# Kernel optimization log

Measured on AMD Instinct MI355X. Metric: run time of the kernel, lower is better.

The kernel has to match this reference:

```python
import jax, jax.numpy as jnp
import numpy as np

N_LAYERS = 4
D_MODEL = 256
P = 128            # ssm_size // 2 (conj_sym S5)
LATENT_DIM = 256
MAX_SEQ_LEN = 32768
OUTPUT_DIM = 64
LN_EPS = 1e-6      # flax nn.LayerNorm default


def layer_norm(x, scale, bias):
    mu = jnp.mean(x, axis=-1, keepdims=True)
    var = jnp.mean(jnp.square(x - mu), axis=-1, keepdims=True)
    return (x - mu) * jax.lax.rsqrt(var + LN_EPS) * scale + bias


def s5_ssm(u, Lre, Lim, Bre, Bim, Cre, Cim, Dvec, log_step, resets):
    """u: (L, H) float. Returns (L, H) float. conj_sym S5, zoh discretization."""
    step = jnp.exp(log_step)                       # (P,)
    Lam = Lre + 1j * Lim                           # (P,) complex
    Lam_bar = jnp.exp(Lam * step)                  # (P,)
    B_bar = ((Lam_bar - 1.0) / Lam)[:, None] * (Bre + 1j * Bim)  # (P, H)
    Bu = u @ B_bar.T                               # (L, P) complex
    A = jnp.broadcast_to(Lam_bar, Bu.shape)        # (L, P)
    c = resets[:, None].astype(u.dtype)            # (L, 1)

    def binop(qi, qj):
        Ai, bi, ci = qi
        Aj, bj, cj = qj
        return (Aj * Ai * (1.0 - cj) + Aj * cj,
                (Aj * bi + bj) * (1.0 - cj) + bj * cj,
                ci * (1.0 - cj) + cj)

    # zero initial hidden state => no prepend needed (identical result)
    _, xs, _ = jax.lax.associative_scan(binop, (A, Bu, c))
    y = 2.0 * jnp.real(xs @ (Cre + 1j * Cim).T)    # (L, H), conj_sym doubling
    return y + u * Dvec


def setup_inputs() -> dict:
    key = jax.random.key(0)
    ks = jax.random.split(key, 16)
    f = jax.random.normal
    return {
        "latent": f(ks[0], (LATENT_DIM,), jnp.float32),
        "W_expand": f(ks[1], (LATENT_DIM, D_MODEL), jnp.float32) / np.sqrt(LATENT_DIM),
        "b_expand": jnp.zeros((D_MODEL,), jnp.float32),
        "norm_scale": jnp.ones((N_LAYERS, D_MODEL), jnp.float32),
        "norm_bias": jnp.zeros((N_LAYERS, D_MODEL), jnp.float32),
        "Lambda_re": -(0.1 + 0.9 * jax.random.uniform(ks[2], (N_LAYERS, P))),
        "Lambda_im": np.pi * f(ks[3], (N_LAYERS, P), jnp.float32),
        "B_re": f(ks[4], (N_LAYERS, P, D_MODEL), jnp.float32) / np.sqrt(D_MODEL),
        "B_im": f(ks[5], (N_LAYERS, P, D_MODEL), jnp.float32) / np.sqrt(D_MODEL),
        "C_re": f(ks[6], (N_LAYERS, D_MODEL, P), jnp.float32) / np.sqrt(P),
        "C_im": f(ks[7], (N_LAYERS, D_MODEL, P), jnp.float32) / np.sqrt(P),
        "D": f(ks[8], (N_LAYERS, D_MODEL), jnp.float32),
        "log_step": jnp.log(jax.random.uniform(ks[9], (N_LAYERS, P), minval=1e-3, maxval=1e-1)),
        "W1": f(ks[10], (N_LAYERS, D_MODEL, D_MODEL), jnp.float32) / np.sqrt(D_MODEL),
        "b1": jnp.zeros((N_LAYERS, D_MODEL), jnp.float32),
        "W2": f(ks[11], (N_LAYERS, D_MODEL, D_MODEL), jnp.float32) / np.sqrt(D_MODEL),
        "b2": jnp.zeros((N_LAYERS, D_MODEL), jnp.float32),
        "W_out": f(ks[12], (D_MODEL, OUTPUT_DIM), jnp.float32) / np.sqrt(D_MODEL),
        "b_out": jnp.zeros((OUTPUT_DIM,), jnp.float32),
        "seq_len": MAX_SEQ_LEN,
    }


def reference(latent, W_expand, b_expand, norm_scale, norm_bias,
              Lambda_re, Lambda_im, B_re, B_im, C_re, C_im, D, log_step,
              W1, b1, W2, b2, W_out, b_out, seq_len):
    # latent_expand + leaky_relu, then broadcast to full trajectory
    x = jax.nn.leaky_relu(latent @ W_expand + b_expand)        # (H,)
    x = jnp.broadcast_to(x[None, :], (MAX_SEQ_LEN, D_MODEL))    # (L, H); batch dim of 1 dropped
    resets = jnp.zeros((MAX_SEQ_LEN,), x.dtype)                 # dones = zeros
    for i in range(N_LAYERS):
        skip = x
        h = layer_norm(x, norm_scale[i], norm_bias[i])          # prenorm
        y = s5_ssm(h, Lambda_re[i], Lambda_im[i], B_re[i], B_im[i],
                   C_re[i], C_im[i], D[i], log_step[i], resets)
        y = layer_norm(y, norm_scale[i], norm_bias[i])          # gtrxl norm (shared params)
        y = jax.nn.gelu(y)
        y = (y @ W1[i] + b1[i]) * jax.nn.sigmoid(y @ W2[i] + b2[i])  # full_glu
        x = skip + y
    return x @ W_out + b_out                                    # (L, output_dim)
```

## Files before the change

### kernel.cpp

```cpp
#include <hip/hip_runtime.h>
#include <stdint.h>

#define LSEQ 32768
#define NCH 512
#define TCH 64

typedef _Float16 half8 __attribute__((ext_vector_type(8)));
typedef _Float16 half4v __attribute__((ext_vector_type(4)));
typedef _Float16 half2v __attribute__((ext_vector_type(2)));
typedef float f32x4 __attribute__((ext_vector_type(4)));
typedef float f32x2 __attribute__((ext_vector_type(2)));

__device__ __forceinline__ float sigmoidf_(float x) { return 1.f / (1.f + __expf(-x)); }
__device__ __forceinline__ float gelu_(float x) {
    float z = 0.7978845608028654f * (x + 0.044715f * x * x * x);
    float e = __expf(2.f * z);
    float t = 1.f - 2.f / (e + 1.f);
    return 0.5f * x * (1.f + t);
}

__device__ __forceinline__ void gll16(const _Float16* gp, _Float16* lp) {
    __builtin_amdgcn_global_load_lds((__attribute__((address_space(1))) void*)gp,
                                     (__attribute__((address_space(3))) void*)lp, 16, 0, 0);
}

__global__ __launch_bounds__(512) void s5_k0a(const float* __restrict__ lre, const float* __restrict__ lim,
                                              const float* __restrict__ lstep,
                                              float* aR, float* aI, float* cbR, float* cbI,
                                              float* aTR, float* aTI, float* alp, float* ralp) {
    int i = threadIdx.x;
    float st = expf(lstep[i]);
    float lr = lre[i] * st, li = lim[i] * st;
    float ea = expf(lr);
    float ar = ea * cosf(li), ai = ea * sinf(li);
    float den = lre[i] * lre[i] + lim[i] * lim[i];
    float nr = ar - 1.f, ni = ai;
    float cr = (nr * lre[i] + ni * lim[i]) / den;
    float ci = (ni * lre[i] - nr * lim[i]) / den;
    float cm = sqrtf(cr * cr + ci * ci);
    float al = sqrtf(2.83f / fmaxf(cm, 1e-8f));
    float eT = expf(lr * (float)TCH);
    aR[i] = ar; aI[i] = ai;
    cbR[i] = cr; cbI[i] = ci;
    aTR[i] = eT * cosf(li * (float)TCH);
    aTI[i] = eT * sinf(li * (float)TCH);
    alp[i] = al; ralp[i] = 1.f / al;
}

__global__ __launch_bounds__(256) void s5_k0b(const float* __restrict__ Bre, const float* __restrict__ Bim,
                                              const float* __restrict__ Cre, const float* __restrict__ Cim,
                                              const float* __restrict__ W1, const float* __restrict__ W2,
                                              const float* __restrict__ b1, const float* __restrict__ b2,
                                              const float* __restrict__ Wout,
                                              const float* __restrict__ cbR, const float* __restrict__ cbI,
                                              const float* __restrict__ alp, const float* __restrict__ ralp,
                                              _Float16* Wbu, _Float16* Wc, _Float16* Wglu,
                                              _Float16* WoutT, float* bglu) {
    int stride = gridDim.x * blockDim.x;
    int tid0 = blockIdx.x * blockDim.x + threadIdx.x;
    for (int i = tid0; i < 262144; i += stride) {
        int l = i >> 16, n = (i >> 8) & 255, k = i & 255;
        int s = n >> 4, lmn = n & 15;
        int p = l * 128 + (s >> 1) * 16 + lmn;
        float re = cbR[p] * Bre[p * 256 + k] - cbI[p] * Bim[p * 256 + k];
        float im = cbR[p] * Bim[p * 256 + k] + cbI[p] * Bre[p * 256 + k];
        Wbu[i] = (_Float16)(((s & 1) ? im : re) * alp[p]);
    }
    for (int i = tid0; i < 262144; i += stride) {
        int l = i >> 16, n = (i >> 8) & 255, k = i & 255;
        int p = k >> 1;
        float base = (k & 1) ? -2.f * Cim[(l * 256 + n) * 128 + p]
                             : 2.f * Cre[(l * 256 + n) * 128 + p];
        Wc[i] = (_Float16)(base * ralp[l * 128 + p]);
    }
    for (int i = tid0; i < 524288; i += stride) {
        int l = i >> 17, n = (i >> 8) & 511, k = i & 255;
        int j = ((n >> 7) << 6) | (((n >> 6) & 1) << 5) | (((n >> 5) & 1) << 4) | (n & 15);
        const float* src = ((n >> 4) & 1) ? W2 : W1;
        Wglu[i] = (_Float16)src[(l * 256 + k) * 256 + j];
    }
    for (int i = tid0; i < 16384; i += stride) {
        int n = i >> 8, k = i & 255;
        WoutT[i] = (_Float16)Wout[k * 64 + n];
    }
    for (int i = tid0; i < 2048; i += stride) {
        int l = i >> 9, n = i & 511;
        int j = ((n >> 7) << 6) | (((n >> 6) & 1) << 5) | (((n >> 5) & 1) << 4) | (n & 15);
        bglu[i] = (((n >> 4) & 1) ? b2 : b1)[l * 256 + j];
    }
}

__global__ __launch_bounds__(256) void s5_k0c(const float* __restrict__ latent, const float* __restrict__ W,
                                              const float* __restrict__ b, _Float16* __restrict__ x0h) {
    __shared__ float lat[256];
    lat[threadIdx.x] = latent[threadIdx.x];
    __syncthreads();
    float s = b[threadIdx.x];
    for (int k = 0; k < 256; ++k) s += lat[k] * W[k * 256 + threadIdx.x];
    x0h[threadIdx.x] = (_Float16)((s > 0.f) ? s : 0.01f * s);
}

__global__ __launch_bounds__(256) void s5_k1_fill(const _Float16* __restrict__ x0h, _Float16* __restrict__ x) {
    int i = blockIdx.x * 256 + threadIdx.x;
    half8 v = *(const half8*)(x0h + (i & 31) * 8);
    *(half8*)(x + i * 8) = v;
}

__global__ __launch_bounds__(512, 1) void s5_k3_lngemm(const _Float16* __restrict__ x,
                                                       const _Float16* __restrict__ Wt,
                                                       const float* __restrict__ gamma,
                                                       const float* __restrict__ beta,
                                                       _Float16* __restrict__ h,
                                                       _Float16* __restrict__ Buh) {
    __shared__ _Float16 sW[128 * 512];
    int tid = threadIdx.x, wid = tid >> 6, lane = tid & 63;
    int lm = lane & 15, quad = lane >> 4;
    int m0 = blockIdx.x * 128;
    int rowb = m0 + wid * 16;

#pragma unroll
    for (int half = 0; half < 2; ++half)
#pragma unroll
        for (int i = 0; i < 8; ++i) {
            int c = i * 8 + wid;
            int ks = c >> 3, n16 = c & 7;
            gll16(Wt + (half * 128 + n16 * 16 + lm) * 256 + ks * 32 + quad * 8,
                  sW + half * 32768 + c * 512);
        }

    int row = rowb + lm;
    half8 af[8];
    {
        half8 xv[8];
#pragma unroll
        for (int ks = 0; ks < 8; ++ks)
            xv[ks] = *(const half8*)(x + row * 256 + ks * 32 + quad * 8);
        float s1 = 0.f, s2 = 0.f;
#pragma unroll
        for (int i = 0; i < 8; ++i)
#pragma unroll
            for (int j = 0; j < 8; ++j) { float t = (float)xv[i][j]; s1 += t; s2 += t * t; }
        s1 += __shfl_xor(s1, 16, 64); s2 += __shfl_xor(s2, 16, 64);
        s1 += __shfl_xor(s1, 32, 64); s2 += __shfl_xor(s2, 32, 64);
        float mu = s1 * (1.f / 256.f);
        float var = s2 * (1.f / 256.f) - mu * mu;
        float rs = rsqrtf(fmaxf(var, 0.f) + 1e-6f);
#pragma unroll
        for (int ks = 0; ks < 8; ++ks) {
            f32x4 g0 = *(const f32x4*)(gamma + ks * 32 + quad * 8);
            f32x4 g1 = *(const f32x4*)(gamma + ks * 32 + quad * 8 + 4);
            f32x4 b0 = *(const f32x4*)(beta + ks * 32 + quad * 8);
            f32x4 b1 = *(const f32x4*)(beta + ks * 32 + quad * 8 + 4);
            half8 o;
#pragma unroll
            for (int j = 0; j < 4; ++j) {
                o[j]     = (_Float16)(((float)xv[ks][j] - mu) * rs * g0[j] + b0[j]);
                o[j + 4] = (_Float16)(((float)xv[ks][j + 4] - mu) * rs * g1[j] + b1[j]);
            }
            af[ks] = o;
            *(half8*)(h + row * 256 + ks * 32 + quad * 8) = o;
        }
    }
    asm volatile("s_waitcnt vmcnt(0)" ::: "memory");
    __syncthreads();

    f32x4 zero = {0.f, 0.f, 0.f, 0.f};
    f32x4 acc[2][8];
#pragma unroll
    for (int hf = 0; hf < 2; ++hf)
#pragma unroll
        for (int nt = 0; nt < 8; ++nt) acc[hf][nt] = zero;

#pragma unroll
    for (int hf = 0; hf < 2; ++hf)
#pragma unroll
        for (int ks = 0; ks < 8; ++ks) {
            half8 bf[8];
#pragma unroll
            for (int nt = 0; nt < 8; ++nt)
                bf[nt] = *(const half8*)(sW + hf * 32768 + (ks * 8 + nt) * 512 + lane * 8);
#pragma unroll
            for (int nt = 0; nt < 8; ++nt)
                acc[hf][nt] = __builtin_amdgcn_mfma_f32_16x16x32_f16(af[ks], bf[nt], acc[hf][nt], 0, 0, 0);
        }

#pragma unroll
    for (int u = 0; u < 8; ++u) {
        int hf = u >> 2, q = u & 3;
        int p = u * 16 + lm;
#pragma unroll
        for (int r = 0; r < 4; ++r) {
            half2v o = {(_Float16)acc[hf][2 * q][r], (_Float16)acc[hf][2 * q + 1][r]};
            *(half2v*)(Buh + (rowb + quad * 4 + r) * 256 + 2 * p) = o;
        }
    }
}

__global__ __launch_bounds__(128, 4) void s5_k4_carry(const _Float16* __restrict__ Bu,
                                                      const float* __restrict__ aR, const float* __restrict__ aI,
                                                      float* __restrict__ carRI) {
    int p = threadIdx.x, c = blockIdx.x;
    int t0 = c * TCH;
    const _Float16* bp = Bu + t0 * 256 + 2 * p;
    half2v hv[TCH];
#pragma unroll
    for (int j = 0; j < TCH; ++j) hv[j] = *(const half2v*)(bp + j * 256);
    float ar = aR[p], ai = aI[p];
    float sr = 0.f, si = 0.f;
#pragma unroll
    for (int j = 0; j < TCH; ++j) {
        float nr = fmaf(ar, sr, fmaf(-ai, si, (float)hv[j][0]));
        float ni = fmaf(ar, si, fmaf(ai, sr, (float)hv[j][1]));
        sr = nr; si = ni;
    }
    *(f32x2*)(carRI + (c * 128 + p) * 2) = f32x2{sr, si};
}

__global__ __launch_bounds__(512, 1) void s5_k7_mega(const _Float16* __restrict__ Bu,
                                                     const float* __restrict__ carRI,
                                                     const _Float16* __restrict__ Wc,
                                                     const _Float16* __restrict__ Wglu,
                                                     const _Float16* __restrict__ h,
                                                     const float* __restrict__ aR, const float* __restrict__ aI,
                                                     const float* __restrict__ aTR, const float* __restrict__ aTI,
                                                     const float* __restrict__ Dv,
                                                     const float* __restrict__ gamma,
                                                     const float* __restrict__ beta,
                                                     const float* __restrict__ bias,
                                                     _Float16* __restrict__ x) {
    __shared__ _Float16 sW[64 * 512];
    __shared__ _Float16 xsT[128 * 256];
    int tid = threadIdx.x, wid = tid >> 6, lane = tid & 63;
    int lm = lane & 15, quad = lane >> 4;
    int m0 = blockIdx.x * 128;
    int rowb = m0 + wid * 16;

    auto stageWc = [&](int half) {
#pragma unroll
        for (int i = 0; i < 8; ++i) {
            int c = i * 8 + wid;
            int ks = c >> 3, n16 = c & 7;
            gll16(Wc + (half * 128 + n16 * 16 + lm) * 256 + ks * 32 + quad * 8, sW + c * 512);
        }
    };
    auto stageWg = [&](int n0) {
#pragma unroll
        for (int i = 0; i < 8; ++i) {
            int c = i * 8 + wid;
            int ks = c >> 3, n16 = c & 7;
            gll16(Wglu + (n0 + n16 * 16 + lm) * 256 + ks * 32 + quad * 8, sW + c * 512);
        }
    };
    stageWc(0);

    if (tid < 256) {
        int cc = tid >> 7, p = tid & 127;
        int cg = blockIdx.x * 2 + cc;
        const _Float16* bp = Bu + (m0 + cc * TCH) * 256 + 2 * p;
        half2v hv[TCH];
#pragma unroll
        for (int j = 0; j < TCH; ++j) hv[j] = *(const half2v*)(bp + j * 256);
        float tr = aTR[p], ti = aTI[p];
        float cr = 0.f, ci = 0.f;
#pragma unroll 8
        for (int i = 0; i < cg; ++i) {
            f32x2 w = *(const f32x2*)(carRI + (i * 128 + p) * 2);
            float nr = fmaf(tr, cr, fmaf(-ti, ci, w[0]));
            float ni = fmaf(tr, ci, fmaf(ti, cr, w[1]));
            cr = nr; ci = ni;
        }
        float ar = aR[p], ai = aI[p];
        float sr = cr, si = ci;
#pragma unroll
        for (int j = 0; j < TCH; ++j) {
            float nr = fmaf(ar, sr, fmaf(-ai, si, (float)hv[j][0]));
            float ni = fmaf(ar, si, fmaf(ai, sr, (float)hv[j][1]));
            sr = nr; si = ni;
            int rl = cc * TCH + j;
            int byte = (4 * p) ^ ((rl & 7) << 4);
            *(half2v*)((char*)xsT + rl * 512 + byte) = half2v{(_Float16)sr, (_Float16)si};
        }
    }
    asm volatile("s_waitcnt vmcnt(0)" ::: "memory");
    __syncthreads();

    int rl = wid * 16 + lm;
    half8 af[8];
#pragma unroll
    for (int ks = 0; ks < 8; ++ks) {
        int b = ks * 64 + quad * 16;
        af[ks] = *(const half8*)((const char*)xsT + rl * 512 + (b ^ ((rl & 7) << 4)));
    }

    f32x4 zero = {0.f, 0.f, 0.f, 0.f};
    f32x4 acc[2][8];
#pragma unroll
    for (int hf = 0; hf < 2; ++hf)
#pragma unroll
        for (int nt = 0; nt < 8; ++nt) acc[hf][nt] = zero;

#pragma unroll
    for (int ks = 0; ks < 8; ++ks) {
        half8 bf[8];
#pragma unroll
        for (int nt = 0; nt < 8; ++nt)
            bf[nt] = *(const half8*)(sW + (ks * 8 + nt) * 512 + lane * 8);
#pragma unroll
        for (int nt = 0; nt < 8; ++nt)
            acc[0][nt] = __builtin_amdgcn_mfma_f32_16x16x32_f16(af[ks], bf[nt], acc[0][nt], 0, 0, 0);
    }
    __syncthreads();
    stageWc(1);
    asm volatile("s_waitcnt vmcnt(0)" ::: "memory");
    __syncthreads();
#pragma unroll
    for (int ks = 0; ks < 8; ++ks) {
        half8 bf[8];
#pragma unroll
        for (int nt = 0; nt < 8; ++nt)
            bf[nt] = *(const half8*)(sW + (ks * 8 + nt) * 512 + lane * 8);
#pragma unroll
        for (int nt = 0; nt < 8; ++nt)
            acc[1][nt] = __builtin_amdgcn_mfma_f32_16x16x32_f16(af[ks], bf[nt], acc[1][nt], 0, 0, 0);
    }

#pragma unroll
    for (int hf = 0; hf < 2; ++hf)
#pragma unroll
        for (int nt = 0; nt < 8; ++nt) {
            int col = hf * 128 + nt * 16 + lm;
            float dv = Dv[col];
#pragma unroll
            for (int r = 0; r < 4; ++r)
                acc[hf][nt][r] += (float)h[(rowb + quad * 4 + r) * 256 + col] * dv;
        }
    float mu[4], rs[4];
#pragma unroll
    for (int r = 0; r < 4; ++r) {
        float a = 0.f, b = 0.f;
#pragma unroll
        for (int hf = 0; hf < 2; ++hf)
#pragma unroll
            for (int nt = 0; nt < 8; ++nt) {
                float v = acc[hf][nt][r];
                a += v; b += v * v;
            }
#pragma unroll
        for (int off = 1; off < 16; off <<= 1) {
            a += __shfl_xor(a, off, 64);
            b += __shfl_xor(b, off, 64);
        }
        float m = a * (1.f / 256.f);
        float var = b * (1.f / 256.f) - m * m;
        mu[r] = m;
        rs[r] = rsqrtf(fmaxf(var, 0.f) + 1e-6f);
    }
#pragma unroll
    for (int hf = 0; hf < 2; ++hf)
#pragma unroll
        for (int nt = 0; nt < 8; ++nt) {
            int col = hf * 128 + nt * 16 + lm;
            float ga = gamma[col], be = beta[col];
#pragma unroll
            for (int r = 0; r < 4; ++r) {
                float hn = (acc[hf][nt][r] - mu[r]) * rs[r] * ga + be;
                int rg = wid * 16 + quad * 4 + r;
                int byte = (2 * col) ^ ((rg & 7) << 4);
                *((_Float16*)((char*)xsT + rg * 512 + byte)) = (_Float16)gelu_(hn);
            }
        }
    __syncthreads();
    stageWg(0);
    half8 ag[8];
#pragma unroll
    for (int ks = 0; ks < 8; ++ks) {
        int b = ks * 64 + quad * 16;
        ag[ks] = *(const half8*)((const char*)xsT + rl * 512 + (b ^ ((rl & 7) << 4)));
    }
    asm volatile("s_waitcnt vmcnt(0)" ::: "memory");
    __syncthreads();

#pragma unroll
    for (int cy = 0; cy < 4; ++cy) {
        f32x4 accg[8];
#pragma unroll
        for (int nt = 0; nt < 8; ++nt) accg[nt] = zero;
#pragma unroll
        for (int ks = 0; ks < 8; ++ks) {
            half8 bf[8];
#pragma unroll
            for (int nt = 0; nt < 8; ++nt)
                bf[nt] = *(const half8*)(sW + (ks * 8 + nt) * 512 + lane * 8);
#pragma unroll
            for (int nt = 0; nt < 8; ++nt)
                accg[nt] = __builtin_amdgcn_mfma_f32_16x16x32_f16(ag[ks], bf[nt], accg[nt], 0, 0, 0);
        }
        int n0 = cy * 128;
        int jbase = (n0 >> 1) + lm;
        _Float16 xold[4][4];
#pragma unroll
        for (int q = 0; q < 4; ++q)
#pragma unroll
            for (int r = 0; r < 4; ++r)
                xold[q][r] = x[(rowb + quad * 4 + r) * 256 + jbase + q * 16];
#pragma unroll
        for (int q = 0; q < 4; ++q) {
            float b1v = bias[n0 + (2 * q) * 16 + lm];
            float b2v = bias[n0 + (2 * q + 1) * 16 + lm];
            int jcol = jbase + q * 16;
#pragma unroll
            for (int r = 0; r < 4; ++r) {
                float u1 = accg[2 * q][r] + b1v;
                float u2 = accg[2 * q + 1][r] + b2v;
                float gl = u1 * sigmoidf_(u2);
                int idx = (rowb + quad * 4 + r) * 256 + jcol;
                x[idx] = (_Float16)((float)xold[q][r] + gl);
            }
        }
        if (cy < 3) {
            __syncthreads();
            stageWg((cy + 1) * 128);
            asm volatile("s_waitcnt vmcnt(0)" ::: "memory");
            __syncthreads();
        }
    }
}

__global__ __launch_bounds__(256, 2) void s5_k9_gemm_out(const _Float16* __restrict__ A,
                                                         const _Float16* __restrict__ Wt,
                                                         const float* __restrict__ bout,
                                                         float* __restrict__ out) {
    __shared__ _Float16 sW[32 * 512];
    int tid = threadIdx.x, wid = tid >> 6, lane = tid & 63;
    int lm = lane & 15, quad = lane >> 4;
    int m0 = blockIdx.x * 128;
#pragma unroll
    for (int i = 0; i < 8; ++i) {
        int c = i * 4 + wid;
        int ks = c >> 2, n16 = c & 3;
        gll16(Wt + (n16 * 16 + lm) * 256 + ks * 32 + quad * 8, sW + c * 512);
    }
    int rowb = m0 + wid * 32;
    half8 af[2][8];
#pragma unroll
    for (int mt = 0; mt < 2; ++mt)
#pragma unroll
        for (int ks = 0; ks < 8; ++ks)
            af[mt][ks] = *(const half8*)(A + (rowb + mt * 16 + lm) * 256 + ks * 32 + quad * 8);
    asm volatile("s_waitcnt vmcnt(0)" ::: "memory");
    __syncthreads();

    f32x4 zero = {0.f, 0.f, 0.f, 0.f};
    f32x4 acc[2][4];
#pragma unroll
    for (int mt = 0; mt < 2; ++mt)
#pragma unroll
        for (int nt = 0; nt < 4; ++nt) acc[mt][nt] = zero;
#pragma unroll
    for (int ks = 0; ks < 8; ++ks) {
        half8 bf[4];
#pragma unroll
        for (int nt = 0; nt < 4; ++nt)
            bf[nt] = *(const half8*)(sW + (ks * 4 + nt) * 512 + lane * 8);
#pragma unroll
        for (int mt = 0; mt < 2; ++mt)
#pragma unroll
            for (int nt = 0; nt < 4; ++nt)
                acc[mt][nt] = __builtin_amdgcn_mfma_f32_16x16x32_f16(af[mt][ks], bf[nt], acc[mt][nt], 0, 0, 0);
    }
#pragma unroll
    for (int mt = 0; mt < 2; ++mt)
#pragma unroll
        for (int nt = 0; nt < 4; ++nt) {
            int col = nt * 16 + lm;
            float bv = bout[col];
#pragma unroll
            for (int r = 0; r < 4; ++r) {
                int row = rowb + mt * 16 + quad * 4 + r;
                out[row * 64 + col] = acc[mt][nt][r] + bv;
            }
        }
}

constexpr size_t OFF_X    = 0;
constexpr size_t OFF_BU   = 33554432;
constexpr size_t OFF_H    = 67108864;
constexpr size_t OFF_WBU  = 100663296;
constexpr size_t OFF_WC   = OFF_WBU + 524288;
constexpr size_t OFF_WGLU = OFF_WC + 524288;
constexpr size_t OFF_WOUT = OFF_WGLU + 1048576;
constexpr size_t OFF_BGLU = OFF_WOUT + 32768;
constexpr size_t OFF_AR   = OFF_BGLU + 8192;
constexpr size_t OFF_AI   = OFF_AR + 2048;
constexpr size_t OFF_CBR  = OFF_AI + 2048;
constexpr size_t OFF_CBI  = OFF_CBR + 2048;
constexpr size_t OFF_ATR  = OFF_CBI + 2048;
constexpr size_t OFF_ATI  = OFF_ATR + 2048;
constexpr size_t OFF_ALP  = OFF_ATI + 2048;
constexpr size_t OFF_RALP = OFF_ALP + 2048;
constexpr size_t OFF_X0H  = OFF_RALP + 2048;
constexpr size_t OFF_CARRI= OFF_X0H + 1024;

extern "C" void kernel_launch(void* const* d_in, const int* in_sizes, int n_in,
                              void* d_out, int out_size, void* d_ws, size_t ws_size,
                              hipStream_t stream) {
    (void)in_sizes; (void)n_in; (void)out_size; (void)ws_size;
    const float* latent    = (const float*)d_in[0];
    const float* W_expand  = (const float*)d_in[1];
    const float* b_expand  = (const float*)d_in[2];
    const float* norm_s    = (const float*)d_in[3];
    const float* norm_b    = (const float*)d_in[4];
    const float* Lre       = (const float*)d_in[5];
    const float* Lim       = (const float*)d_in[6];
    const float* Bre       = (const float*)d_in[7];
    const float* Bim       = (const float*)d_in[8];
    const float* Cre       = (const float*)d_in[9];
    const float* Cim       = (const float*)d_in[10];
    const float* Dv        = (const float*)d_in[11];
    const float* lstep     = (const float*)d_in[12];
    const float* W1        = (const float*)d_in[13];
    const float* b1        = (const float*)d_in[14];
    const float* W2        = (const float*)d_in[15];
    const float* b2        = (const float*)d_in[16];
    const float* Wout      = (const float*)d_in[17];
    const float* bout      = (const float*)d_in[18];

    char* ws = (char*)d_ws;
    _Float16* x    = (_Float16*)(ws + OFF_X);
    _Float16* Buh  = (_Float16*)(ws + OFF_BU);
    _Float16* hbuf = (_Float16*)(ws + OFF_H);
    _Float16* Wbu  = (_Float16*)(ws + OFF_WBU);
    _Float16* Wc   = (_Float16*)(ws + OFF_WC);
    _Float16* Wglu = (_Float16*)(ws + OFF_WGLU);
    _Float16* WoutT= (_Float16*)(ws + OFF_WOUT);
    float* bglu = (float*)(ws + OFF_BGLU);
    float* aR  = (float*)(ws + OFF_AR);
    float* aI  = (float*)(ws + OFF_AI);
    float* cbR = (float*)(ws + OFF_CBR);
    float* cbI = (float*)(ws + OFF_CBI);
    float* aTR = (float*)(ws + OFF_ATR);
    float* aTI = (float*)(ws + OFF_ATI);
    float* alp = (float*)(ws + OFF_ALP);
    float* ralp= (float*)(ws + OFF_RALP);
    _Float16* x0h = (_Float16*)(ws + OFF_X0H);
    float* carRI=(float*)(ws + OFF_CARRI);

    s5_k0a<<<1, 512, 0, stream>>>(Lre, Lim, lstep, aR, aI, cbR, cbI, aTR, aTI, alp, ralp);
    s5_k0b<<<256, 256, 0, stream>>>(Bre, Bim, Cre, Cim, W1, W2, b1, b2, Wout,
                                    cbR, cbI, alp, ralp, Wbu, Wc, Wglu, WoutT, bglu);
    s5_k0c<<<1, 256, 0, stream>>>(latent, W_expand, b_expand, x0h);
    s5_k1_fill<<<4096, 256, 0, stream>>>(x0h, x);

    for (int l = 0; l < 4; ++l) {
        s5_k3_lngemm<<<256, 512, 0, stream>>>(x, Wbu + l * 65536,
                                              norm_s + l * 256, norm_b + l * 256,
                                              hbuf, Buh);
        s5_k4_carry<<<NCH, 128, 0, stream>>>(Buh, aR + l * 128, aI + l * 128, carRI);
        s5_k7_mega<<<256, 512, 0, stream>>>(Buh, carRI, Wc + l * 65536, Wglu + l * 131072,
                                            hbuf,
                                            aR + l * 128, aI + l * 128,
                                            aTR + l * 128, aTI + l * 128,
                                            Dv + l * 256,
                                            norm_s + l * 256, norm_b + l * 256,
                                            bglu + l * 512, x);
    }
    s5_k9_gemm_out<<<256, 256, 0, stream>>>(x, WoutT, bout, (float*)d_out);
}
```

Baseline: 461.1 us.

## Fuse chunk-carry scan into LN+Bu GEMM kernel via LDS-staged Bu tile

```diff
diff --git a/kernel.cpp b/kernel.cpp
--- a/kernel.cpp
+++ b/kernel.cpp
@@ -110,23 +110,27 @@
                                                        const _Float16* __restrict__ Wt,
                                                        const float* __restrict__ gamma,
                                                        const float* __restrict__ beta,
+                                                       const float* __restrict__ aR,
+                                                       const float* __restrict__ aI,
                                                        _Float16* __restrict__ h,
-                                                       _Float16* __restrict__ Buh) {
-    __shared__ _Float16 sW[128 * 512];
+                                                       _Float16* __restrict__ Buh,
+                                                       float* __restrict__ carRI) {
+    __shared__ _Float16 sW[64 * 512];
+    __shared__ _Float16 BuT[128 * 256];
     int tid = threadIdx.x, wid = tid >> 6, lane = tid & 63;
     int lm = lane & 15, quad = lane >> 4;
     int m0 = blockIdx.x * 128;
     int rowb = m0 + wid * 16;
 
-#pragma unroll
-    for (int half = 0; half < 2; ++half)
+    auto stageW = [&](int half) {
 #pragma unroll
         for (int i = 0; i < 8; ++i) {
             int c = i * 8 + wid;
             int ks = c >> 3, n16 = c & 7;
-            gll16(Wt + (half * 128 + n16 * 16 + lm) * 256 + ks * 32 + quad * 8,
-                  sW + half * 32768 + c * 512);
-        }
+            gll16(Wt + (half * 128 + n16 * 16 + lm) * 256 + ks * 32 + quad * 8, sW + c * 512);
+        }
+    };
+    stageW(0);
 
     int row = rowb + lm;
     half8 af[8];
@@ -172,17 +176,29 @@
         for (int nt = 0; nt < 8; ++nt) acc[hf][nt] = zero;
 
 #pragma unroll
-    for (int hf = 0; hf < 2; ++hf)
-#pragma unroll
-        for (int ks = 0; ks < 8; ++ks) {
-            half8 bf[8];
-#pragma unroll
-            for (int nt = 0; nt < 8; ++nt)
-                bf[nt] = *(const half8*)(sW + hf * 32768 + (ks * 8 + nt) * 512 + lane * 8);
-#pragma unroll
-            for (int nt = 0; nt < 8; ++nt)
-                acc[hf][nt] = __builtin_amdgcn_mfma_f32_16x16x32_f16(af[ks], bf[nt], acc[hf][nt], 0, 0, 0);
-        }
+    for (int ks = 0; ks < 8; ++ks) {
+        half8 bf[8];
+#pragma unroll
+        for (int nt = 0; nt < 8; ++nt)
+            bf[nt] = *(const half8*)(sW + (ks * 8 + nt) * 512 + lane * 8);
+#pragma unroll
+        for (int nt = 0; nt < 8; ++nt)
+            acc[0][nt] = __builtin_amdgcn_mfma_f32_16x16x32_f16(af[ks], bf[nt], acc[0][nt], 0, 0, 0);
+    }
+    __syncthreads();
+    stageW(1);
+    asm volatile("s_waitcnt vmcnt(0)" ::: "memory");
+    __syncthreads();
+#pragma unroll
+    for (int ks = 0; ks < 8; ++ks) {
+        half8 bf[8];
+#pragma unroll
+        for (int nt = 0; nt < 8; ++nt)
+            bf[nt] = *(const half8*)(sW + (ks * 8 + nt) * 512 + lane * 8);
+#pragma unroll
+        for (int nt = 0; nt < 8; ++nt)
+            acc[1][nt] = __builtin_amdgcn_mfma_f32_16x16x32_f16(af[ks], bf[nt], acc[1][nt], 0, 0, 0);
+    }
 
 #pragma unroll
     for (int u = 0; u < 8; ++u) {
@@ -191,29 +207,32 @@
 #pragma unroll
         for (int r = 0; r < 4; ++r) {
             half2v o = {(_Float16)acc[hf][2 * q][r], (_Float16)acc[hf][2 * q + 1][r]};
-            *(half2v*)(Buh + (rowb + quad * 4 + r) * 256 + 2 * p) = o;
-        }
-    }
-}
-
-__global__ __launch_bounds__(128, 4) void s5_k4_carry(const _Float16* __restrict__ Bu,
-                                                      const float* __restrict__ aR, const float* __restrict__ aI,
-                                                      float* __restrict__ carRI) {
-    int p = threadIdx.x, c = blockIdx.x;
-    int t0 = c * TCH;
-    const _Float16* bp = Bu + t0 * 256 + 2 * p;
-    half2v hv[TCH];
-#pragma unroll
-    for (int j = 0; j < TCH; ++j) hv[j] = *(const half2v*)(bp + j * 256);
-    float ar = aR[p], ai = aI[p];
-    float sr = 0.f, si = 0.f;
-#pragma unroll
-    for (int j = 0; j < TCH; ++j) {
-        float nr = fmaf(ar, sr, fmaf(-ai, si, (float)hv[j][0]));
-        float ni = fmaf(ar, si, fmaf(ai, sr, (float)hv[j][1]));
-        sr = nr; si = ni;
-    }
-    *(f32x2*)(carRI + (c * 128 + p) * 2) = f32x2{sr, si};
+            int rg = wid * 16 + quad * 4 + r;
+            *(half2v*)(Buh + (m0 + rg) * 256 + 2 * p) = o;
+            int byte = (4 * p) ^ ((rg & 7) << 4);
+            *(half2v*)((char*)BuT + rg * 512 + byte) = o;
+        }
+    }
+    __syncthreads();
+
+    if (tid < 256) {
+        int cc = tid >> 7, p = tid & 127;
+        half2v hv[TCH];
+#pragma unroll
+        for (int j = 0; j < TCH; ++j) {
+            int rl = cc * TCH + j;
+            hv[j] = *(const half2v*)((const char*)BuT + rl * 512 + ((4 * p) ^ ((rl & 7) << 4)));
+        }
+        float ar = aR[p], ai = aI[p];
+        float sr = 0.f, si = 0.f;
+#pragma unroll
+        for (int j = 0; j < TCH; ++j) {
+            float nr = fmaf(ar, sr, fmaf(-ai, si, (float)hv[j][0]));
+            float ni = fmaf(ar, si, fmaf(ai, sr, (float)hv[j][1]));
+            sr = nr; si = ni;
+        }
+        *(f32x2*)(carRI + ((blockIdx.x * 2 + cc) * 128 + p) * 2) = f32x2{sr, si};
+    }
 }
 
 __global__ __launch_bounds__(512, 1) void s5_k7_mega(const _Float16* __restrict__ Bu,
@@ -554,8 +573,8 @@
     for (int l = 0; l < 4; ++l) {
         s5_k3_lngemm<<<256, 512, 0, stream>>>(x, Wbu + l * 65536,
                                               norm_s + l * 256, norm_b + l * 256,
-                                              hbuf, Buh);
-        s5_k4_carry<<<NCH, 128, 0, stream>>>(Buh, aR + l * 128, aI + l * 128, carRI);
+                                              aR + l * 128, aI + l * 128,
+                                              hbuf, Buh, carRI);
         s5_k7_mega<<<256, 512, 0, stream>>>(Buh, carRI, Wc + l * 65536, Wglu + l * 131072,
                                             hbuf,
                                             aR + l * 128, aI + l * 128,
```

Measured after the change: 452.0 us, median of 3. -2.0%, faster.
